# Kernel tuning notes

Measured on AMD Instinct MI355X. Metric: run time of the kernel, lower is better.

The kernel has to match this reference:

```python
import jax, jax.numpy as jnp
import numpy as np

EPS = 1e-8  # torch cosine_similarity norm clamp
TEMP = 1.0

def _gelu(h):
    return jax.nn.gelu(h, approximate=False)  # torch nn.GELU default (erf)

def _layernorm(h, g, b, eps=1e-5):
    mu = jnp.mean(h, axis=-1, keepdims=True)
    var = jnp.var(h, axis=-1, keepdims=True)
    return (h - mu) * jax.lax.rsqrt(var + eps) * g + b

def _encoder(h, eW1, eb1, eW2, eb2, eW3, eb3, ln_g, ln_b):
    h = _gelu(h @ eW1 + eb1)
    h = _gelu(h @ eW2 + eb2)
    h = h @ eW3 + eb3
    return _layernorm(h, ln_g, ln_b)

def _normalize(v):
    n = jnp.sqrt(jnp.sum(v * v, axis=-1, keepdims=True))
    return v / jnp.maximum(n, EPS)

def setup_inputs() -> dict:
    key = jax.random.key(0)
    ks = jax.random.split(key, 8)
    B, D, H, K = 16384, 512, 512, 11
    s = 0.02
    return {
        'x': jax.random.normal(ks[0], (B, D), jnp.float32),
        'tW1': jax.random.normal(ks[1], (K, D, H), jnp.float32) * s,
        'tb1': jnp.zeros((K, H), jnp.float32),
        'tW2': jax.random.normal(ks[2], (K, H, H), jnp.float32) * s,
        'tb2': jnp.zeros((K, H), jnp.float32),
        'tW3': jax.random.normal(ks[3], (K, H, D), jnp.float32) * s,
        'tb3': jnp.zeros((K, D), jnp.float32),
        'eW1': jax.random.normal(ks[4], (D, H), jnp.float32) * s,
        'eb1': jnp.zeros((H,), jnp.float32),
        'eW2': jax.random.normal(ks[5], (H, H), jnp.float32) * s,
        'eb2': jnp.zeros((H,), jnp.float32),
        'eW3': jax.random.normal(ks[6], (H, H), jnp.float32) * s,
        'eb3': jnp.zeros((H,), jnp.float32),
        'ln_g': jnp.ones((H,), jnp.float32),
        'ln_b': jnp.zeros((H,), jnp.float32),
    }

def reference(x, tW1, tb1, tW2, tb2, tW3, tb3, eW1, eb1, eW2, eb2, eW3, eb3, ln_g, ln_b):
    K = tW1.shape[0]
    # K learned transforms, vectorized over k: [K, B, D]
    h = _gelu(jnp.einsum('bi,kij->kbj', x, tW1) + tb1[:, None, :])
    h = _gelu(jnp.einsum('kbi,kij->kbj', h, tW2) + tb2[:, None, :])
    tx = jnp.einsum('kbi,kij->kbj', h, tW3) + tb3[:, None, :]
    # shared encoder on x and on each transformed view
    z = _encoder(x, eW1, eb1, eW2, eb2, eW3, eb3, ln_g, ln_b)      # [B, H]
    zk = _encoder(tx, eW1, eb1, eW2, eb2, eW3, eb3, ln_g, ln_b)    # [K, B, H]
    zn = _normalize(z)
    zkn = _normalize(zk)
    pos = jnp.einsum('bh,kbh->kb', zn, zkn) / TEMP                 # sim(z, z_k)
    S = jnp.einsum('lbh,kbh->lkb', zkn, zkn) / TEMP                # sim(z_l, z_k)
    diag = jnp.eye(K, dtype=bool)[:, :, None]
    Sm = jnp.where(diag, -jnp.inf, S)                              # drop l == k
    all_terms = jnp.concatenate([pos[None], Sm], axis=0)           # [K+1, K, B]
    log_den = jax.nn.logsumexp(all_terms, axis=0)                  # [K, B]
    return -jnp.sum(pos - log_den, axis=0)                         # [B]
```

## Files before the change

kernel.cpp:

```cpp
#include <hip/hip_runtime.h>
#include <hip/hip_bf16.h>
#include <cstdint>

typedef __attribute__((ext_vector_type(8))) short short8;
typedef __attribute__((ext_vector_type(4))) float f32x4;
typedef __attribute__((ext_vector_type(4))) short short4v;

__device__ __forceinline__ float b2f(short s) {
    unsigned u = ((unsigned)(unsigned short)s) << 16;
    return __builtin_bit_cast(float, u);
}
__device__ __forceinline__ short f2b(float f) {
    unsigned u = __builtin_bit_cast(unsigned, f);
    u += 0x7fff + ((u >> 16) & 1);
    return (short)(u >> 16);
}

__device__ __forceinline__ float gelu_t(float x) {
    const float c1 = 2.302184829f;
    const float c2 = 0.102947246f;
    float x2 = x * x;
    float t  = __builtin_fmaf(c2, x2, c1);
    float e  = __builtin_amdgcn_exp2f(x * t);
    return x - __fdividef(x, e + 1.0f);
}

__device__ __forceinline__ void async16(const void* g, void* l) {
    __builtin_amdgcn_global_load_lds(
        (const __attribute__((address_space(1))) unsigned int*)g,
        (__attribute__((address_space(3))) unsigned int*)l, 16, 0, 0);
}

#define BM 128
#define BN 128
#define BKK 64

template<bool GELU>
__global__ __launch_bounds__(256)
void gemm_bt(const short* __restrict__ A, long sA,
             const short* __restrict__ Bt, long sB,
             const float* __restrict__ bias, long sBias,
             short* __restrict__ C, long sC) {
    const int z = blockIdx.z;
    A    += (long)z * sA;
    Bt   += (long)z * sB;
    bias += (long)z * sBias;
    C    += (long)z * sC;

    const int nwg = (int)gridDim.x;
    const int q   = nwg >> 3;
    const int bx  = (int)blockIdx.x;
    const int flat = (bx & 7) * q + (bx >> 3);
    const long arow0 = (long)(flat >> 2) * BM;
    const long brow0 = (long)(flat & 3) * BN;

    __shared__ alignas(16) short smem[2 * BM * BKK];
    short* As = smem;
    short* Bs = smem + BM * BKK;

    const int tid  = threadIdx.x;
    const int lane = tid & 63;
    const int w    = tid >> 6;
    const int wr   = w >> 1, wc = w & 1;
    const int  K = 512;

    f32x4 acc[4][4] = {};

    const int srow = lane >> 3;
    const int scol = ((lane & 7) ^ srow) * 8;

    for (int k0 = 0; k0 < K; k0 += BKK) {
        __syncthreads();
#pragma unroll
        for (int i = 0; i < 4; ++i) {
            const int r0 = (i * 4 + w) * 8;
            async16(A  + (arow0 + r0 + srow) * K + k0 + scol, &As[r0 * BKK]);
            async16(Bt + (brow0 + r0 + srow) * K + k0 + scol, &Bs[r0 * BKK]);
        }
        __syncthreads();
        const int lr = lane & 15;
        const int r7 = lane & 7;
#pragma unroll
        for (int kk = 0; kk < BKK; kk += 32) {
            const int c0 = (kk >> 3) + (lane >> 4);
            short8 a[4], b[4];
#pragma unroll
            for (int m = 0; m < 4; ++m)
                a[m] = *(const short8*)&As[(wr * 64 + m * 16 + lr) * BKK + ((c0 ^ r7) * 8)];
#pragma unroll
            for (int n = 0; n < 4; ++n)
                b[n] = *(const short8*)&Bs[(wc * 64 + n * 16 + lr) * BKK + ((c0 ^ r7) * 8)];
#pragma unroll
            for (int m = 0; m < 4; ++m)
#pragma unroll
                for (int n = 0; n < 4; ++n)
                    acc[m][n] = __builtin_amdgcn_mfma_f32_16x16x32_bf16(
                        a[m], b[n], acc[m][n], 0, 0, 0);
        }
    }

    __syncthreads();
    short* E = smem + w * (32 * 72);
    const int cl = lane & 15;
    const int rl = (lane >> 4) * 4;
#pragma unroll
    for (int h = 0; h < 2; ++h) {
#pragma unroll
        for (int n = 0; n < 4; ++n) {
            const int col = (int)brow0 + wc * 64 + n * 16 + cl;
            const float bs = bias[col];
            const int ecol = n * 16 + cl;
#pragma unroll
            for (int ml = 0; ml < 2; ++ml) {
                const int m = h * 2 + ml;
                float g0 = acc[m][n][0] + bs, g1 = acc[m][n][1] + bs;
                float g2 = acc[m][n][2] + bs, g3 = acc[m][n][3] + bs;
                if (GELU) { g0 = gelu_t(g0); g1 = gelu_t(g1); g2 = gelu_t(g2); g3 = gelu_t(g3); }
                unsigned p01, p23;
                asm("v_cvt_pk_bf16_f32 %0, %1, %2" : "=v"(p01) : "v"(g0), "v"(g1));
                asm("v_cvt_pk_bf16_f32 %0, %1, %2" : "=v"(p23) : "v"(g2), "v"(g3));
                const int r0 = ml * 16 + rl;
                E[(r0 + 0) * 72 + ecol] = (short)(p01 & 0xffff);
                E[(r0 + 1) * 72 + ecol] = (short)(p01 >> 16);
                E[(r0 + 2) * 72 + ecol] = (short)(p23 & 0xffff);
                E[(r0 + 3) * 72 + ecol] = (short)(p23 >> 16);
            }
        }
#pragma unroll
        for (int chunk = 0; chunk < 4; ++chunk) {
            const int rloc = chunk * 8 + (lane >> 3);
            const int c0   = (lane & 7) * 8;
            short8 v = *(const short8*)&E[rloc * 72 + c0];
            *(short8*)&C[(arow0 + wr * 64 + h * 32 + rloc) * 512 + brow0 + wc * 64 + c0] = v;
        }
    }
}

__global__ __launch_bounds__(256)
void transpose_conv(const float* __restrict__ src, short* __restrict__ dst) {
    __shared__ float t[32][33];
    const long moff = (long)blockIdx.z * 512 * 512;
    const float* s = src + moff;
    short* d = dst + moff;
    const int tx = threadIdx.x & 31, ty = threadIdx.x >> 5;
    const int bi = blockIdx.x, bj = blockIdx.y;
#pragma unroll
    for (int j = 0; j < 4; ++j)
        t[ty + j * 8][tx] = s[(long)(bi * 32 + ty + j * 8) * 512 + bj * 32 + tx];
    __syncthreads();
#pragma unroll
    for (int j = 0; j < 4; ++j)
        d[(long)(bj * 32 + ty + j * 8) * 512 + bi * 32 + tx] = f2b(t[tx][ty + j * 8]);
}

__global__ __launch_bounds__(256)
void conv_f32_bf16_2(const float* __restrict__ src, short* __restrict__ d1,
                     short* __restrict__ d2, long n) {
    long i = ((long)blockIdx.x * 256 + threadIdx.x) * 4;
    if (i >= n) return;
    float4 f = *(const float4*)&src[i];
    short4v o;
    o[0] = f2b(f.x); o[1] = f2b(f.y); o[2] = f2b(f.z); o[3] = f2b(f.w);
    *(short4v*)&d1[i] = o;
    *(short4v*)&d2[i] = o;
}

__global__ __launch_bounds__(256)
void ln_loss(const short* __restrict__ H, const float* __restrict__ g,
             const float* __restrict__ bta, float* __restrict__ out, int CH) {
    __shared__ alignas(16) short Z[4][16 * 520];
    const int wid = threadIdx.x >> 6, lane = threadIdx.x & 63;
    const long b = (long)blockIdx.x * 4 + wid;
    short* Zw = &Z[wid][0];

#pragma unroll
    for (int r = 12; r < 16; ++r)
        *(short8*)&Zw[r * 520 + lane * 8] = (short8){0, 0, 0, 0, 0, 0, 0, 0};

    for (int s = 0; s < 12; ++s) {
        short8 t = *(const short8*)&H[((long)s * CH + b) * 512 + lane * 8];
        float v[8];
        float sum = 0.f, ss = 0.f;
#pragma unroll
        for (int j = 0; j < 8; ++j) { v[j] = b2f(t[j]); sum += v[j]; ss += v[j] * v[j]; }
#pragma unroll
        for (int o = 1; o < 64; o <<= 1) { sum += __shfl_xor(sum, o, 64); ss += __shfl_xor(ss, o, 64); }
        const float mu = sum * (1.f / 512.f);
        const float rs = rsqrtf(ss * (1.f / 512.f) - mu * mu + 1e-5f);
        float y[8]; float nsq = 0.f;
#pragma unroll
        for (int j = 0; j < 8; ++j) {
            const int col = lane * 8 + j;
            y[j] = (v[j] - mu) * rs * g[col] + bta[col];
            nsq += y[j] * y[j];
        }
#pragma unroll
        for (int o = 1; o < 64; o <<= 1) nsq += __shfl_xor(nsq, o, 64);
        const float inv = 1.f / fmaxf(sqrtf(nsq), 1e-8f);
        short8 o8;
#pragma unroll
        for (int j = 0; j < 8; ++j) o8[j] = f2b(y[j] * inv);
        *(short8*)&Zw[s * 520 + lane * 8] = o8;
    }

    f32x4 acc = {0.f, 0.f, 0.f, 0.f};
    const int lr = lane & 15, hi = lane >> 4;
#pragma unroll
    for (int st = 0; st < 16; ++st) {
        short8 a = *(const short8*)&Zw[lr * 520 + st * 32 + hi * 8];
        acc = __builtin_amdgcn_mfma_f32_16x16x32_bf16(a, a, acc, 0, 0, 0);
    }
    const int col = lr;
    float lmax = -3.0e38f;
    bool valid[4];
#pragma unroll
    for (int i = 0; i < 4; ++i) {
        const int row = hi * 4 + i;
        valid[i] = (row < 12) && (row != col);
        if (valid[i]) lmax = fmaxf(lmax, acc[i]);
    }
    lmax = fmaxf(lmax, __shfl_xor(lmax, 16, 64));
    lmax = fmaxf(lmax, __shfl_xor(lmax, 32, 64));
    float esum = 0.f;
#pragma unroll
    for (int i = 0; i < 4; ++i)
        if (valid[i]) esum += __builtin_amdgcn_exp2f((acc[i] - lmax) * 1.44269504f);
    esum += __shfl_xor(esum, 16, 64);
    esum += __shfl_xor(esum, 32, 64);
    float contrib = 0.f;
    if (hi == 0 && col >= 1 && col <= 11) {
        const float logden = lmax + __builtin_amdgcn_logf(esum) * 0.6931471806f;
        contrib = acc[0] - logden;
    }
#pragma unroll
    for (int o = 1; o < 16; o <<= 1) contrib += __shfl_xor(contrib, o, 64);
    if (lane == 0) out[b] = -contrib;
}

extern "C" void kernel_launch(void* const* d_in, const int* in_sizes, int n_in,
                              void* d_out, int out_size, void* d_ws, size_t ws_size,
                              hipStream_t stream) {
    const float* x    = (const float*)d_in[0];
    const float* tW1  = (const float*)d_in[1];
    const float* tb1  = (const float*)d_in[2];
    const float* tW2  = (const float*)d_in[3];
    const float* tb2  = (const float*)d_in[4];
    const float* tW3  = (const float*)d_in[5];
    const float* tb3  = (const float*)d_in[6];
    const float* eW1  = (const float*)d_in[7];
    const float* eb1  = (const float*)d_in[8];
    const float* eW2  = (const float*)d_in[9];
    const float* eb2  = (const float*)d_in[10];
    const float* eW3  = (const float*)d_in[11];
    const float* eb3  = (const float*)d_in[12];
    const float* ln_g = (const float*)d_in[13];
    const float* ln_b = (const float*)d_in[14];

    const int  B    = in_sizes[0] / 512;
    const long WMAT = 512L * 512L;

    int  c  = 1;
    long CH = B;
    for (;;) {
        CH = (long)B / c;
        size_t need = (size_t)36 * WMAT * 2 + (size_t)24 * CH * 512 * 2 + 4096;
        if (need <= ws_size || CH <= 256) break;
        c <<= 1;
    }
    const long SLAB = 12L * CH * 512;

    short* wt  = (short*)d_ws;
    short* X12 = wt  + 36L * WMAT;
    short* hA  = X12 + SLAB;

    {
        dim3 tgK(16, 16, 11), tg1(16, 16, 1);
        transpose_conv<<<tgK, 256, 0, stream>>>(tW1, wt + 0L * WMAT);
        transpose_conv<<<tgK, 256, 0, stream>>>(tW2, wt + 11L * WMAT);
        transpose_conv<<<tgK, 256, 0, stream>>>(tW3, wt + 22L * WMAT);
        transpose_conv<<<tg1, 256, 0, stream>>>(eW1, wt + 33L * WMAT);
        transpose_conv<<<tg1, 256, 0, stream>>>(eW2, wt + 34L * WMAT);
        transpose_conv<<<tg1, 256, 0, stream>>>(eW3, wt + 35L * WMAT);
    }

    const long SC = CH * 512;
    const dim3 gT((unsigned)(CH / 32), 1, 11);
    const dim3 gE((unsigned)(3 * CH / 8), 1, 1);

    for (int ch = 0; ch < c; ++ch) {
        conv_f32_bf16_2<<<(unsigned)((SC / 4 + 255) / 256), 256, 0, stream>>>(
            x + (long)ch * SC, X12, hA, SC);

        gemm_bt<true ><<<gT, 256, 0, stream>>>(hA,        0,  wt + 0L * WMAT,  WMAT, tb1, 512, X12 + SC, SC);
        gemm_bt<true ><<<gT, 256, 0, stream>>>(X12 + SC,  SC, wt + 11L * WMAT, WMAT, tb2, 512, hA + SC,  SC);
        gemm_bt<false><<<gT, 256, 0, stream>>>(hA + SC,   SC, wt + 22L * WMAT, WMAT, tb3, 512, X12 + SC, SC);

        gemm_bt<true ><<<gE, 256, 0, stream>>>(X12, 0, wt + 33L * WMAT, 0, eb1, 0, hA,  0);
        gemm_bt<true ><<<gE, 256, 0, stream>>>(hA,  0, wt + 34L * WMAT, 0, eb2, 0, X12, 0);
        gemm_bt<false><<<gE, 256, 0, stream>>>(X12, 0, wt + 35L * WMAT, 0, eb3, 0, hA,  0);

        ln_loss<<<(unsigned)(CH / 4), 256, 0, stream>>>(
            hA, ln_g, ln_b, (float*)d_out + (long)ch * CH, (int)CH);
    }
}
```

Measured before the change: 1.131 ms.

## Enlarge GEMM tiles to 256x256 with 8 waves and triple-buffered async loads

The bf16 GEMM kernel moves from 128x128 tiles with BK=64 and a double-sync loop to 256x256 tiles computed by 512 threads (8 waves, each 128x64). It uses a 3-stage ring of BK=32 LDS buffers, filled by direct global-to-LDS loads, with explicit vmcnt waits so loads for step t+2 overlap the MFMA work for step t. Larger tiles raise arithmetic intensity and halve redundant operand traffic, while the pipeline hides load latency. In exchange there are far fewer workgroups per launch, higher register pressure (32 accumulators per thread), and more LDS per block.

```diff
diff --git a/kernel.cpp b/kernel.cpp
--- a/kernel.cpp
+++ b/kernel.cpp
@@ -31,12 +31,10 @@
         (__attribute__((address_space(3))) unsigned int*)l, 16, 0, 0);
 }
 
-#define BM 128
-#define BN 128
-#define BKK 64
+#define NT 16
 
 template<bool GELU>
-__global__ __launch_bounds__(256)
+__global__ __launch_bounds__(512, 2)
 void gemm_bt(const short* __restrict__ A, long sA,
              const short* __restrict__ Bt, long sB,
              const float* __restrict__ bias, long sBias,
@@ -48,66 +46,80 @@
     C    += (long)z * sC;
 
     const int nwg = (int)gridDim.x;
-    const int q   = nwg >> 3;
     const int bx  = (int)blockIdx.x;
-    const int flat = (bx & 7) * q + (bx >> 3);
-    const long arow0 = (long)(flat >> 2) * BM;
-    const long brow0 = (long)(flat & 3) * BN;
-
-    __shared__ alignas(16) short smem[2 * BM * BKK];
-    short* As = smem;
-    short* Bs = smem + BM * BKK;
+    int flat = bx;
+    if ((nwg & 7) == 0) { const int q = nwg >> 3; flat = (bx & 7) * q + (bx >> 3); }
+    const long arow0 = (long)(flat >> 1) * 256;
+    const long brow0 = (long)(flat & 1) * 256;
+
+    __shared__ alignas(16) short smem[3 * 16384];
 
     const int tid  = threadIdx.x;
     const int lane = tid & 63;
     const int w    = tid >> 6;
-    const int wr   = w >> 1, wc = w & 1;
-    const int  K = 512;
-
-    f32x4 acc[4][4] = {};
-
-    const int srow = lane >> 3;
-    const int scol = ((lane & 7) ^ srow) * 8;
-
-    for (int k0 = 0; k0 < K; k0 += BKK) {
-        __syncthreads();
-#pragma unroll
-        for (int i = 0; i < 4; ++i) {
-            const int r0 = (i * 4 + w) * 8;
-            async16(A  + (arow0 + r0 + srow) * K + k0 + scol, &As[r0 * BKK]);
-            async16(Bt + (brow0 + r0 + srow) * K + k0 + scol, &Bs[r0 * BKK]);
-        }
-        __syncthreads();
-        const int lr = lane & 15;
-        const int r7 = lane & 7;
-#pragma unroll
-        for (int kk = 0; kk < BKK; kk += 32) {
-            const int c0 = (kk >> 3) + (lane >> 4);
-            short8 a[4], b[4];
-#pragma unroll
-            for (int m = 0; m < 4; ++m)
-                a[m] = *(const short8*)&As[(wr * 64 + m * 16 + lr) * BKK + ((c0 ^ r7) * 8)];
+    const int wrow = w >> 2, wcol = w & 3;
+    const int lr = lane & 15, hi = lane >> 4;
+
+    f32x4 acc[8][4] = {};
+
+    const int rl4 = lane >> 2;
+    const int sc  = ((lane & 3) ^ (rl4 & 3)) * 8;
+
+    auto stage = [&](int q, int t) {
+        short* Ab = smem + q * 16384;
+        short* Bb = Ab + 8192;
+        const int k0 = t * 32;
+#pragma unroll
+        for (int j = 0; j < 2; ++j) {
+            const int rbase = j * 128 + w * 16;
+            async16(A  + (arow0 + rbase + rl4) * 512 + k0 + sc, Ab + rbase * 32);
+            async16(Bt + (brow0 + rbase + rl4) * 512 + k0 + sc, Bb + rbase * 32);
+        }
+    };
+
+    stage(0, 0);
+    stage(1, 1);
+
+#pragma unroll
+    for (int t = 0; t < NT; ++t) {
+        if (t + 2 < NT) stage((t + 2) % 3, t + 2);
+        if (t + 2 < NT)      asm volatile("s_waitcnt vmcnt(8)" ::: "memory");
+        else if (t + 1 < NT) asm volatile("s_waitcnt vmcnt(4)" ::: "memory");
+        else                 asm volatile("s_waitcnt vmcnt(0)" ::: "memory");
+        __builtin_amdgcn_sched_barrier(0);
+        __builtin_amdgcn_s_barrier();
+        __builtin_amdgcn_sched_barrier(0);
+
+        const short* Ab = smem + (t % 3) * 16384;
+        const short* Bb = Ab + 8192;
+        short8 a[8], b[4];
+#pragma unroll
+        for (int n = 0; n < 4; ++n) {
+            const int r = wcol * 64 + n * 16 + lr;
+            b[n] = *(const short8*)&Bb[r * 32 + ((hi ^ (lr & 3)) * 8)];
+        }
+#pragma unroll
+        for (int m = 0; m < 8; ++m) {
+            const int r = wrow * 128 + m * 16 + lr;
+            a[m] = *(const short8*)&Ab[r * 32 + ((hi ^ (lr & 3)) * 8)];
+        }
+#pragma unroll
+        for (int m = 0; m < 8; ++m)
 #pragma unroll
             for (int n = 0; n < 4; ++n)
-                b[n] = *(const short8*)&Bs[(wc * 64 + n * 16 + lr) * BKK + ((c0 ^ r7) * 8)];
-#pragma unroll
-            for (int m = 0; m < 4; ++m)
-#pragma unroll
-                for (int n = 0; n < 4; ++n)
-                    acc[m][n] = __builtin_amdgcn_mfma_f32_16x16x32_bf16(
-                        a[m], b[n], acc[m][n], 0, 0, 0);
-        }
-    }
-
-    __syncthreads();
+                acc[m][n] = __builtin_amdgcn_mfma_f32_16x16x32_bf16(
+                    a[m], b[n], acc[m][n], 0, 0, 0);
+
+        __builtin_amdgcn_s_barrier();
+    }
+
     short* E = smem + w * (32 * 72);
-    const int cl = lane & 15;
-    const int rl = (lane >> 4) * 4;
-#pragma unroll
-    for (int h = 0; h < 2; ++h) {
+    const int cl = lr, rl = hi * 4;
+#pragma unroll
+    for (int h = 0; h < 4; ++h) {
 #pragma unroll
         for (int n = 0; n < 4; ++n) {
-            const int col = (int)brow0 + wc * 64 + n * 16 + cl;
+            const int col = (int)brow0 + wcol * 64 + n * 16 + cl;
             const float bs = bias[col];
             const int ecol = n * 16 + cl;
 #pragma unroll
@@ -131,7 +143,8 @@
             const int rloc = chunk * 8 + (lane >> 3);
             const int c0   = (lane & 7) * 8;
             short8 v = *(const short8*)&E[rloc * 72 + c0];
-            *(short8*)&C[(arow0 + wr * 64 + h * 32 + rloc) * 512 + brow0 + wc * 64 + c0] = v;
+            *(short8*)&C[(arow0 + wrow * 128 + h * 32 + rloc) * 512
+                         + brow0 + wcol * 64 + c0] = v;
         }
     }
 }
@@ -284,20 +297,20 @@
     }
 
     const long SC = CH * 512;
-    const dim3 gT((unsigned)(CH / 32), 1, 11);
-    const dim3 gE((unsigned)(3 * CH / 8), 1, 1);
+    const dim3 gT((unsigned)(CH / 256 * 2), 1, 11);
+    const dim3 gE((unsigned)(12 * CH / 256 * 2), 1, 1);
 
     for (int ch = 0; ch < c; ++ch) {
         conv_f32_bf16_2<<<(unsigned)((SC / 4 + 255) / 256), 256, 0, stream>>>(
             x + (long)ch * SC, X12, hA, SC);
 
-        gemm_bt<true ><<<gT, 256, 0, stream>>>(hA,        0,  wt + 0L * WMAT,  WMAT, tb1, 512, X12 + SC, SC);
-        gemm_bt<true ><<<gT, 256, 0, stream>>>(X12 + SC,  SC, wt + 11L * WMAT, WMAT, tb2, 512, hA + SC,  SC);
-        gemm_bt<false><<<gT, 256, 0, stream>>>(hA + SC,   SC, wt + 22L * WMAT, WMAT, tb3, 512, X12 + SC, SC);
-
-        gemm_bt<true ><<<gE, 256, 0, stream>>>(X12, 0, wt + 33L * WMAT, 0, eb1, 0, hA,  0);
-        gemm_bt<true ><<<gE, 256, 0, stream>>>(hA,  0, wt + 34L * WMAT, 0, eb2, 0, X12, 0);
-        gemm_bt<false><<<gE, 256, 0, stream>>>(X12, 0, wt + 35L * WMAT, 0, eb3, 0, hA,  0);
+        gemm_bt<true ><<<gT, 512, 0, stream>>>(hA,        0,  wt + 0L * WMAT,  WMAT, tb1, 512, X12 + SC, SC);
+        gemm_bt<true ><<<gT, 512, 0, stream>>>(X12 + SC,  SC, wt + 11L * WMAT, WMAT, tb2, 512, hA + SC,  SC);
+        gemm_bt<false><<<gT, 512, 0, stream>>>(hA + SC,   SC, wt + 22L * WMAT, WMAT, tb3, 512, X12 + SC, SC);
+
+        gemm_bt<true ><<<gE, 512, 0, stream>>>(X12, 0, wt + 33L * WMAT, 0, eb1, 0, hA,  0);
+        gemm_bt<true ><<<gE, 512, 0, stream>>>(hA,  0, wt + 34L * WMAT, 0, eb2, 0, X12, 0);
+        gemm_bt<false><<<gE, 512, 0, stream>>>(X12, 0, wt + 35L * WMAT, 0, eb3, 0, hA,  0);
 
         ln_loss<<<(unsigned)(CH / 4), 256, 0, stream>>>(
             hA, ln_g, ln_b, (float*)d_out + (long)ch * CH, (int)CH);
```

After: 1.054 ms. 1.07x faster.
